# Kernel optimization log

Hardware: AMD Instinct MI355X
Metric: run time of the kernel (lower is better)

The kernel has to match this reference:

```python
import jax, jax.numpy as jnp
import numpy as np
from jax import lax

R, BS, NATM, NORB = 2, 128, 81, 240
M_DIM = 16


def _init(key, shape, scale=0.05):
    return (jax.random.normal(key, shape) * scale).astype(jnp.float32)


def setup_inputs() -> dict:
    key = jax.random.key(0)
    ks = jax.random.split(key, 24)
    return {
        "xyz": jax.random.normal(ks[0], (R, BS, NATM, 3), jnp.float32) * 3.0,
        "cn": jax.random.uniform(ks[1], (R, BS, NATM), jnp.float32),
        "edisp": jax.random.normal(ks[2], (R, BS, NATM), jnp.float32),
        "ovlp": jax.random.normal(ks[3], (R, BS, NORB, NORB), jnp.float32),
        "h0": jax.random.normal(ks[4], (R, BS, NORB, NORB), jnp.float32),
        "egfn1": jax.random.normal(ks[5], (R, BS), jnp.float32),
        "nu": jax.random.normal(ks[6], (BS, R), jnp.float32),
        # EGNN(dim=2): edge_input_dim = 2*dim + 1 = 5
        "We1": _init(ks[7], (10, 5)), "be1": jnp.zeros((10,), jnp.float32),
        "We2": _init(ks[8], (M_DIM, 10)), "be2": jnp.zeros((M_DIM,), jnp.float32),
        "Wc1": _init(ks[9], (M_DIM * 4, M_DIM)), "bc1": jnp.zeros((M_DIM * 4,), jnp.float32),
        "Wc2": _init(ks[10], (1, M_DIM * 4)), "bc2": jnp.zeros((1,), jnp.float32),
        "coors_scale": jnp.full((1,), 1e-2, jnp.float32),
        "Wn1": _init(ks[11], (4, 2 + M_DIM)), "bn1": jnp.zeros((4,), jnp.float32),
        "Wn2": _init(ks[12], (2, 4)), "bn2": jnp.zeros((2,), jnp.float32),
        "conv1_w": _init(ks[13], (2, 1, 2, 2), 0.2), "conv1_b": jnp.zeros((2,), jnp.float32),
        "conv2_w": _init(ks[14], (2, 2, 2, 2), 0.2), "conv2_b": jnp.zeros((2,), jnp.float32),
        "fc1_w": _init(ks[15], (60, 14087), 0.01), "fc1_b": jnp.zeros((60,), jnp.float32),
        "fc2_w": _init(ks[16], (30, 60)), "fc2_b": jnp.zeros((30,), jnp.float32),
        "fc3_w": _init(ks[17], (1, 30)), "fc3_b": jnp.zeros((1,), jnp.float32),
    }


def _egnn(feats, coors, We1, be1, We2, be2, Wc1, bc1, Wc2, bc2, scale, Wn1, bn1, Wn2, bn2):
    # feats: (b, n, 2), coors: (b, n, 3); dense all-pairs EGNN layer (lucidrains defaults)
    b, n, d = feats.shape
    rel = coors[:, :, None, :] - coors[:, None, :, :]            # (b, i, j, 3)
    rel_dist = jnp.sum(rel * rel, axis=-1, keepdims=True)        # (b, i, j, 1) squared dist
    fi = jnp.broadcast_to(feats[:, :, None, :], (b, n, n, d))
    fj = jnp.broadcast_to(feats[:, None, :, :], (b, n, n, d))
    edge_in = jnp.concatenate([fi, fj, rel_dist], axis=-1)       # (b, i, j, 5)
    m = jax.nn.silu(edge_in @ We1.T + be1)
    m = jax.nn.silu(m @ We2.T + be2)                             # (b, i, j, M_DIM)
    cw = (jax.nn.silu(m @ Wc1.T + bc1) @ Wc2.T + bc2)[..., 0]    # (b, i, j)
    # CoorsNorm: unit-normalize rel coords, learned scale (init 1e-2)
    norm = jnp.sqrt(jnp.clip(rel_dist, 1e-16, None))
    rel_n = rel / norm * scale
    coors_out = jnp.einsum('bij,bijc->bic', cw, rel_n) + coors
    m_i = jnp.sum(m, axis=2)                                     # sum pooling over j
    node_in = jnp.concatenate([feats, m_i], axis=-1)
    feats_out = jax.nn.silu(node_in @ Wn1.T + bn1) @ Wn2.T + bn2 + feats
    return feats_out, coors_out


def _maxpool2(x):
    return lax.reduce_window(x, -jnp.inf, lax.max, (1, 1, 2, 2), (1, 1, 2, 2), 'VALID')


def _conv_block(x, w1, b1, w2, b2):
    # x: (b, N, N) -> NCHW conv stack matching conv1/pool/conv2/pool
    x = x[:, None, :, :]
    x = lax.conv_general_dilated(x, w1, (1, 1), 'VALID', dimension_numbers=('NCHW', 'OIHW', 'NCHW'))
    x = _maxpool2(jax.nn.leaky_relu(x + b1[None, :, None, None]))
    x = lax.conv_general_dilated(x, w2, (1, 1), 'VALID', dimension_numbers=('NCHW', 'OIHW', 'NCHW'))
    x = _maxpool2(jax.nn.leaky_relu(x + b2[None, :, None, None]))
    return x


def reference(xyz, cn, edisp, ovlp, h0, egfn1, nu,
              We1, be1, We2, be2, Wc1, bc1, Wc2, bc2, coors_scale,
              Wn1, bn1, Wn2, bn2, conv1_w, conv1_b, conv2_w, conv2_b,
              fc1_w, fc1_b, fc2_w, fc2_b, fc3_w, fc3_b):
    contribs = []
    for i in range(R):  # fixed small reactant list, mirrors the Python loop
        feats = jnp.stack([cn[i], edisp[i]], axis=-1)            # (bs, n_atms, 2)
        atm, _ = _egnn(feats, xyz[i], We1, be1, We2, be2, Wc1, bc1, Wc2, bc2,
                       coors_scale, Wn1, bn1, Wn2, bn2)
        o = _conv_block(ovlp[i], conv1_w, conv1_b, conv2_w, conv2_b)
        h = _conv_block(h0[i], conv1_w, conv1_b, conv2_w, conv2_b)
        x = jnp.concatenate([o, h], axis=1).reshape(o.shape[0], -1)   # (bs, 4*59*59)
        x = jnp.concatenate([x, atm.reshape(atm.shape[0], -1), egfn1[i][:, None]], axis=1)
        x = jax.nn.leaky_relu(x @ fc1_w.T + fc1_b)
        x = jax.nn.leaky_relu(x @ fc2_w.T + fc2_b)
        x = x @ fc3_w.T + fc3_b                                   # (bs, 1)
        contribs.append(x * nu[:, i][:, None])
    return jnp.sum(jnp.concatenate(contribs, axis=1), axis=1)    # (bs,)
```

## Files before the change

### kernel.cpp

```cpp
#include <hip/hip_runtime.h>
#include <hip/hip_bf16.h>

#define XDIM 14087
#define NATM 81
#define BS   128
#define KC   128
#define NKCH 111

__device__ __forceinline__ float fast_rcp(float x) {
    return __builtin_amdgcn_rcpf(x);
}
__device__ __forceinline__ float silu(float z) {
    return z * fast_rcp(1.f + __expf(-z));
}
__device__ __forceinline__ float leaky(float z) {
    return (z > 0.f) ? z : 0.01f * z;
}

__global__ __launch_bounds__(512) void egnn_kernel(
    const float* __restrict__ xyz, const float* __restrict__ cn,
    const float* __restrict__ edisp, const float* __restrict__ egfn1,
    const float* __restrict__ We1, const float* __restrict__ be1,
    const float* __restrict__ We2, const float* __restrict__ be2,
    const float* __restrict__ Wn1, const float* __restrict__ bn1,
    const float* __restrict__ Wn2, const float* __restrict__ bn2,
    float* __restrict__ xbuf)
{
    const int bid = blockIdx.x;
    const int tid = threadIdx.x;

    __shared__ float sc[NATM][3];
    __shared__ float sf[NATM][2];
    __shared__ float sai[NATM][10];
    __shared__ float sbj[NATM][10];
    __shared__ float sW2[160];
    __shared__ float sbe2[16];
    __shared__ float sw5[10];
    __shared__ float sWn1[72];
    __shared__ float sbn1[4];
    __shared__ float sWn2[8];
    __shared__ float sbn2[2];
    __shared__ float smp[3][NATM][17];

    const float* xb = xyz + (size_t)bid * NATM * 3;
    for (int idx = tid; idx < NATM * 3; idx += 512) sc[idx / 3][idx % 3] = xb[idx];
    if (tid < NATM) {
        const float f0 = cn[(size_t)bid * NATM + tid];
        const float f1 = edisp[(size_t)bid * NATM + tid];
        sf[tid][0] = f0; sf[tid][1] = f1;
        #pragma unroll
        for (int k = 0; k < 10; ++k) {
            sai[tid][k] = be1[k] + We1[k * 5 + 0] * f0 + We1[k * 5 + 1] * f1;
            sbj[tid][k] =          We1[k * 5 + 2] * f0 + We1[k * 5 + 3] * f1;
        }
    }
    if (tid < 160) sW2[tid] = We2[tid];
    if (tid < 16)  sbe2[tid] = be2[tid];
    if (tid < 10)  sw5[tid] = We1[tid * 5 + 4];
    if (tid < 72)  sWn1[tid] = Wn1[tid];
    if (tid < 4)   sbn1[tid] = bn1[tid];
    if (tid < 8)   sWn2[tid] = Wn2[tid];
    if (tid < 2)   sbn2[tid] = bn2[tid];
    __syncthreads();

    if (tid < 486) {
        const int i    = tid % 81;
        const int part = (tid / 81) % 3;
        const int half = tid / 243;

        float W2r[80];
        #pragma unroll
        for (int q = 0; q < 80; ++q) W2r[q] = sW2[half * 80 + q];
        float be2r[8];
        #pragma unroll
        for (int q = 0; q < 8; ++q) be2r[q] = sbe2[half * 8 + q];
        float w5r[10];
        #pragma unroll
        for (int k = 0; k < 10; ++k) w5r[k] = sw5[k];
        float air[10];
        #pragma unroll
        for (int k = 0; k < 10; ++k) air[k] = sai[i][k];
        const float ci0 = sc[i][0], ci1 = sc[i][1], ci2 = sc[i][2];

        float macc[8];
        #pragma unroll
        for (int q = 0; q < 8; ++q) macc[q] = 0.f;

        const int j0 = part * 27;
        for (int j = j0; j < j0 + 27; ++j) {
            const float dx = ci0 - sc[j][0];
            const float dy = ci1 - sc[j][1];
            const float dz = ci2 - sc[j][2];
            const float rd = dx * dx + dy * dy + dz * dz;
            float h[10];
            #pragma unroll
            for (int k = 0; k < 10; ++k) {
                const float z = air[k] + sbj[j][k] + w5r[k] * rd;
                h[k] = silu(z);
            }
            #pragma unroll
            for (int q = 0; q < 8; ++q) {
                float z = be2r[q];
                #pragma unroll
                for (int k = 0; k < 10; ++k) z += W2r[q * 10 + k] * h[k];
                macc[q] += silu(z);
            }
        }
        #pragma unroll
        for (int q = 0; q < 8; ++q) smp[part][i][half * 8 + q] = macc[q];
    }
    __syncthreads();

    if (tid < NATM) {
        float mi[16];
        #pragma unroll
        for (int q = 0; q < 16; ++q)
            mi[q] = smp[0][tid][q] + smp[1][tid][q] + smp[2][tid][q];
        const float f0 = sf[tid][0], f1 = sf[tid][1];
        float n1[4];
        #pragma unroll
        for (int k = 0; k < 4; ++k) {
            float z = sbn1[k] + sWn1[k * 18 + 0] * f0 + sWn1[k * 18 + 1] * f1;
            #pragma unroll
            for (int q = 0; q < 16; ++q) z += sWn1[k * 18 + 2 + q] * mi[q];
            n1[k] = silu(z);
        }
        float* xrow = xbuf + (size_t)bid * XDIM + 13924 + tid * 2;
        #pragma unroll
        for (int c = 0; c < 2; ++c) {
            float z = sbn2[c] + (c ? f1 : f0);
            #pragma unroll
            for (int k = 0; k < 4; ++k) z += sWn2[c * 4 + k] * n1[k];
            xrow[c] = z;
        }
    }
    if (tid == 0) xbuf[(size_t)bid * XDIM + 14086] = egfn1[bid];
}

__global__ __launch_bounds__(256) void conv_kernel(
    const float* __restrict__ ovlp, const float* __restrict__ h0,
    const float* __restrict__ w1, const float* __restrict__ b1,
    const float* __restrict__ w2, const float* __restrict__ b2,
    float* __restrict__ xbuf)
{
    const int bid   = blockIdx.x;
    const int strip = bid % 15;
    const int img   = bid / 15;
    const int b     = img & 127;
    const int t     = (img >> 7) & 1;
    const int r     = img >> 8;
    const int tid   = threadIdx.x;

    const int wv = tid >> 6;
    const int l  = tid & 63;
    const int y  = strip * 4 + wv;
    if (y >= 59) return;
    const int x  = l;
    const int xc = (x < 59) ? x : 59;

    const float* src = (t ? h0 : ovlp) + (size_t)(r * BS + b) * 57600;

    float w1r[8], w2r[16], b1r[2], b2r[2];
    #pragma unroll
    for (int k = 0; k < 8; ++k) w1r[k] = w1[k];
    #pragma unroll
    for (int k = 0; k < 16; ++k) w2r[k] = w2[k];
    b1r[0] = b1[0]; b1r[1] = b1[1];
    b2r[0] = b2[0]; b2r[1] = b2[1];

    float P[7][5];
    #pragma unroll
    for (int rr = 0; rr < 7; ++rr) {
        const float* rp = src + (4 * y + rr) * 240 + 4 * xc;
        const float4 a = *reinterpret_cast<const float4*>(rp);
        P[rr][0] = a.x; P[rr][1] = a.y; P[rr][2] = a.z; P[rr][3] = a.w;
        P[rr][4] = rp[4];
    }

    float p1o[2][3][2];
    #pragma unroll
    for (int c = 0; c < 2; ++c) {
        const float wa = w1r[c * 4 + 0], wb = w1r[c * 4 + 1];
        const float wc = w1r[c * 4 + 2], wd = w1r[c * 4 + 3];
        const float bb = b1r[c];
        #pragma unroll
        for (int pr = 0; pr < 3; ++pr)
        #pragma unroll
        for (int pc = 0; pc < 2; ++pc) {
            float mx = -3.4e38f;
            #pragma unroll
            for (int s = 0; s < 2; ++s)
            #pragma unroll
            for (int tt = 0; tt < 2; ++tt) {
                const int u = 2 * pr + s, v = 2 * pc + tt;
                const float raw = fmaf(wa, P[u][v], fmaf(wb, P[u][v + 1],
                                  fmaf(wc, P[u + 1][v], fmaf(wd, P[u + 1][v + 1], bb))));
                mx = fmaxf(mx, raw);
            }
            p1o[c][pr][pc] = leaky(mx);
        }
    }

    float p1[2][3][3];
    #pragma unroll
    for (int c = 0; c < 2; ++c)
    #pragma unroll
    for (int pr = 0; pr < 3; ++pr) {
        p1[c][pr][0] = p1o[c][pr][0];
        p1[c][pr][1] = p1o[c][pr][1];
        p1[c][pr][2] = __shfl_down(p1o[c][pr][0], 1);
    }

    if (x < 59) {
        float* xrow = xbuf + (size_t)(r * BS + b) * XDIM + (size_t)(t * 2) * 3481
                      + y * 59 + x;
        #pragma unroll
        for (int c2 = 0; c2 < 2; ++c2) {
            float mx = -3.4e38f;
            #pragma unroll
            for (int a2 = 0; a2 < 2; ++a2)
            #pragma unroll
            for (int b2i = 0; b2i < 2; ++b2i) {
                float acc = b2r[c2];
                #pragma unroll
                for (int c1 = 0; c1 < 2; ++c1)
                #pragma unroll
                for (int du = 0; du < 2; ++du)
                #pragma unroll
                for (int dv = 0; dv < 2; ++dv)
                    acc += w2r[((c2 * 2 + c1) * 2 + du) * 2 + dv]
                         * p1[c1][a2 + du][b2i + dv];
                mx = fmaxf(mx, acc);
            }
            xrow[(size_t)c2 * 3481] = leaky(mx);
        }
    }
}

__global__ __launch_bounds__(256) void gemm_fc1_kernel(
    const float* __restrict__ xbuf, const float* __restrict__ fc1w,
    float* __restrict__ psum)
{
    const int kc   = blockIdx.x;
    const int mt   = blockIdx.y;
    const int tid  = threadIdx.x;
    const int kbase = kc * KC;
    const int rem   = min(KC, XDIM - kbase);
    const int row0  = mt * 32;

    __shared__ float4 X4[32][33];
    __shared__ float4 W4[64][33];

    float* Xs = reinterpret_cast<float*>(&X4[0][0]);
    float* Ws = reinterpret_cast<float*>(&W4[0][0]);

    for (int idx = tid; idx < 32 * KC; idx += 256) {
        const int m = idx >> 7, k = idx & 127;
        Xs[m * 132 + k] = (k < rem) ? xbuf[(size_t)(row0 + m) * XDIM + kbase + k] : 0.f;
    }
    for (int idx = tid; idx < 64 * KC; idx += 256) {
        const int n = idx >> 7, k = idx & 127;
        Ws[n * 132 + k] = (n < 60 && k < rem) ? fc1w[(size_t)n * XDIM + kbase + k] : 0.f;
    }
    __syncthreads();

    const int ty = tid >> 4, tx = tid & 15;
    const int m0 = ty * 2;

    float acc[2][4];
    #pragma unroll
    for (int i = 0; i < 2; ++i)
    #pragma unroll
    for (int j = 0; j < 4; ++j) acc[i][j] = 0.f;

    #pragma unroll 4
    for (int k4 = 0; k4 < 32; ++k4) {
        const float4 xa = X4[m0][k4];
        const float4 xb = X4[m0 + 1][k4];
        #pragma unroll
        for (int j = 0; j < 4; ++j) {
            const float4 w = W4[tx + 16 * j][k4];
            acc[0][j] += xa.x * w.x + xa.y * w.y + xa.z * w.z + xa.w * w.w;
            acc[1][j] += xb.x * w.x + xb.y * w.y + xb.z * w.z + xb.w * w.w;
        }
    }

    float* po = psum + ((size_t)kc * 256 + row0) * 64;
    #pragma unroll
    for (int i = 0; i < 2; ++i)
    #pragma unroll
    for (int j = 0; j < 4; ++j)
        po[(size_t)(m0 + i) * 64 + tx + 16 * j] = acc[i][j];
}

__global__ __launch_bounds__(512) void fc_tail_kernel(
    const float* __restrict__ psum,
    const float* __restrict__ fc1b,
    const float* __restrict__ fc2w, const float* __restrict__ fc2b,
    const float* __restrict__ fc3w, const float* __restrict__ fc3b,
    const float* __restrict__ nu, float* __restrict__ out)
{
    const int b = blockIdx.x;
    const int tid = threadIdx.x;
    const int n  = tid & 63;
    const int kq = (tid >> 6) & 3;
    const int rh = tid >> 8;

    __shared__ float red[2][4][64];
    __shared__ float y1s[2][64];
    __shared__ float y2s[2][30];

    const int row = rh * 128 + b;
    float s = 0.f;
    for (int kcc = kq; kcc < NKCH; kcc += 4)
        s += psum[((size_t)kcc * 256 + row) * 64 + n];
    red[rh][kq][n] = s;
    __syncthreads();

    if (kq == 0) {
        float t = red[rh][0][n] + red[rh][1][n] + red[rh][2][n] + red[rh][3][n];
        y1s[rh][n] = (n < 60) ? leaky(t + fc1b[n]) : 0.f;
    }
    __syncthreads();

    if (kq == 0 && n < 30) {
        float a2 = fc2b[n];
        const float* wr = fc2w + n * 60;
        #pragma unroll
        for (int k = 0; k < 60; ++k) a2 += wr[k] * y1s[rh][k];
        y2s[rh][n] = leaky(a2);
    }
    __syncthreads();

    if (tid == 0) {
        float acc_out = 0.f;
        #pragma unroll
        for (int r = 0; r < 2; ++r) {
            float a3 = fc3b[0];
            #pragma unroll
            for (int k = 0; k < 30; ++k) a3 += fc3w[k] * y2s[r][k];
            acc_out += a3 * nu[b * 2 + r];
        }
        out[b] = acc_out;
    }
}

extern "C" void kernel_launch(void* const* d_in, const int* in_sizes, int n_in,
                              void* d_out, int out_size, void* d_ws, size_t ws_size,
                              hipStream_t stream)
{
    const float* xyz   = (const float*)d_in[0];
    const float* cn    = (const float*)d_in[1];
    const float* edisp = (const float*)d_in[2];
    const float* ovlp  = (const float*)d_in[3];
    const float* h0    = (const float*)d_in[4];
    const float* egfn1 = (const float*)d_in[5];
    const float* nu    = (const float*)d_in[6];
    const float* We1   = (const float*)d_in[7];
    const float* be1   = (const float*)d_in[8];
    const float* We2   = (const float*)d_in[9];
    const float* be2   = (const float*)d_in[10];
    const float* Wn1   = (const float*)d_in[16];
    const float* bn1   = (const float*)d_in[17];
    const float* Wn2   = (const float*)d_in[18];
    const float* bn2   = (const float*)d_in[19];
    const float* c1w   = (const float*)d_in[20];
    const float* c1b   = (const float*)d_in[21];
    const float* c2w   = (const float*)d_in[22];
    const float* c2b   = (const float*)d_in[23];
    const float* fc1w  = (const float*)d_in[24];
    const float* fc1b  = (const float*)d_in[25];
    const float* fc2w  = (const float*)d_in[26];
    const float* fc2b  = (const float*)d_in[27];
    const float* fc3w  = (const float*)d_in[28];
    const float* fc3b  = (const float*)d_in[29];

    float* xbuf = (float*)d_ws;
    float* psum = (float*)((char*)d_ws + 14425088);
    float* out  = (float*)d_out;

    hipLaunchKernelGGL(egnn_kernel, dim3(256), dim3(512), 0, stream,
                       xyz, cn, edisp, egfn1, We1, be1, We2, be2,
                       Wn1, bn1, Wn2, bn2, xbuf);
    hipLaunchKernelGGL(conv_kernel, dim3(2 * 2 * BS * 15), dim3(256), 0, stream,
                       ovlp, h0, c1w, c1b, c2w, c2b, xbuf);
    hipLaunchKernelGGL(gemm_fc1_kernel, dim3(NKCH, 8), dim3(256), 0, stream,
                       xbuf, fc1w, psum);
    hipLaunchKernelGGL(fc_tail_kernel, dim3(128), dim3(512), 0, stream,
                       psum, fc1b, fc2w, fc2b, fc3w, fc3b, nu, out);
}
```

Measured before the change: 272.4 us.

## Pad activation rows, use direct global-to-LDS loads with XOR swizzle, two rows per conv wave

New measurement: 248.7 us. 1.1x faster.

```diff
diff --git a/kernel.cpp b/kernel.cpp
--- a/kernel.cpp
+++ b/kernel.cpp
@@ -2,6 +2,7 @@
 #include <hip/hip_bf16.h>
 
 #define XDIM 14087
+#define XPAD 14208
 #define NATM 81
 #define BS   128
 #define KC   128
@@ -15,6 +16,19 @@
 }
 __device__ __forceinline__ float leaky(float z) {
     return (z > 0.f) ? z : 0.01f * z;
+}
+
+__device__ __forceinline__ void gload_lds16(const float* g, float* l) {
+    __builtin_amdgcn_global_load_lds(
+        (const __attribute__((address_space(1))) unsigned int*)g,
+        (__attribute__((address_space(3))) unsigned int*)l, 16, 0, 0);
+}
+
+__global__ __launch_bounds__(128) void padzero_kernel(float* __restrict__ xbuf) {
+    const int row = blockIdx.x;
+    const int tid = threadIdx.x;
+    if (tid < XPAD - XDIM)
+        xbuf[(size_t)row * XPAD + XDIM + tid] = 0.f;
 }
 
 __global__ __launch_bounds__(512) void egnn_kernel(
@@ -125,7 +139,7 @@
             for (int q = 0; q < 16; ++q) z += sWn1[k * 18 + 2 + q] * mi[q];
             n1[k] = silu(z);
         }
-        float* xrow = xbuf + (size_t)bid * XDIM + 13924 + tid * 2;
+        float* xrow = xbuf + (size_t)bid * XPAD + 13924 + tid * 2;
         #pragma unroll
         for (int c = 0; c < 2; ++c) {
             float z = sbn2[c] + (c ? f1 : f0);
@@ -134,7 +148,7 @@
             xrow[c] = z;
         }
     }
-    if (tid == 0) xbuf[(size_t)bid * XDIM + 14086] = egfn1[bid];
+    if (tid == 0) xbuf[(size_t)bid * XPAD + 14086] = egfn1[bid];
 }
 
 __global__ __launch_bounds__(256) void conv_kernel(
@@ -144,8 +158,8 @@
     float* __restrict__ xbuf)
 {
     const int bid   = blockIdx.x;
-    const int strip = bid % 15;
-    const int img   = bid / 15;
+    const int strip = bid & 7;
+    const int img   = bid >> 3;
     const int b     = img & 127;
     const int t     = (img >> 7) & 1;
     const int r     = img >> 8;
@@ -153,8 +167,8 @@
 
     const int wv = tid >> 6;
     const int l  = tid & 63;
-    const int y  = strip * 4 + wv;
-    if (y >= 59) return;
+    const int y0 = strip * 8 + wv * 2;
+    if (y0 >= 59) return;
     const int x  = l;
     const int xc = (x < 59) ? x : 59;
 
@@ -168,23 +182,26 @@
     b1r[0] = b1[0]; b1r[1] = b1[1];
     b2r[0] = b2[0]; b2r[1] = b2[1];
 
-    float P[7][5];
-    #pragma unroll
-    for (int rr = 0; rr < 7; ++rr) {
-        const float* rp = src + (4 * y + rr) * 240 + 4 * xc;
-        const float4 a = *reinterpret_cast<const float4*>(rp);
+    float P[11][5];
+    #pragma unroll
+    for (int rr = 0; rr < 11; ++rr) {
+        int gr = 4 * y0 + rr;
+        if (gr > 239) gr = 239;
+        const float4 a = *reinterpret_cast<const float4*>(src + gr * 240 + 4 * xc);
         P[rr][0] = a.x; P[rr][1] = a.y; P[rr][2] = a.z; P[rr][3] = a.w;
-        P[rr][4] = rp[4];
-    }
-
-    float p1o[2][3][2];
+    }
+    #pragma unroll
+    for (int rr = 0; rr < 11; ++rr)
+        P[rr][4] = __shfl_down(P[rr][0], 1);
+
+    float p1o[2][5][2];
     #pragma unroll
     for (int c = 0; c < 2; ++c) {
         const float wa = w1r[c * 4 + 0], wb = w1r[c * 4 + 1];
         const float wc = w1r[c * 4 + 2], wd = w1r[c * 4 + 3];
         const float bb = b1r[c];
         #pragma unroll
-        for (int pr = 0; pr < 3; ++pr)
+        for (int pr = 0; pr < 5; ++pr)
         #pragma unroll
         for (int pc = 0; pc < 2; ++pc) {
             float mx = -3.4e38f;
@@ -201,38 +218,43 @@
         }
     }
 
-    float p1[2][3][3];
+    float p1[2][5][3];
     #pragma unroll
     for (int c = 0; c < 2; ++c)
     #pragma unroll
-    for (int pr = 0; pr < 3; ++pr) {
+    for (int pr = 0; pr < 5; ++pr) {
         p1[c][pr][0] = p1o[c][pr][0];
         p1[c][pr][1] = p1o[c][pr][1];
         p1[c][pr][2] = __shfl_down(p1o[c][pr][0], 1);
     }
 
-    if (x < 59) {
-        float* xrow = xbuf + (size_t)(r * BS + b) * XDIM + (size_t)(t * 2) * 3481
-                      + y * 59 + x;
-        #pragma unroll
-        for (int c2 = 0; c2 < 2; ++c2) {
-            float mx = -3.4e38f;
-            #pragma unroll
-            for (int a2 = 0; a2 < 2; ++a2)
-            #pragma unroll
-            for (int b2i = 0; b2i < 2; ++b2i) {
-                float acc = b2r[c2];
+    #pragma unroll
+    for (int oy = 0; oy < 2; ++oy) {
+        const int y = y0 + oy;
+        if (y >= 59) break;
+        if (x < 59) {
+            float* xrow = xbuf + (size_t)(r * BS + b) * XPAD + (size_t)(t * 2) * 3481
+                          + y * 59 + x;
+            #pragma unroll
+            for (int c2 = 0; c2 < 2; ++c2) {
+                float mx = -3.4e38f;
                 #pragma unroll
-                for (int c1 = 0; c1 < 2; ++c1)
+                for (int a2 = 0; a2 < 2; ++a2)
                 #pragma unroll
-                for (int du = 0; du < 2; ++du)
-                #pragma unroll
-                for (int dv = 0; dv < 2; ++dv)
-                    acc += w2r[((c2 * 2 + c1) * 2 + du) * 2 + dv]
-                         * p1[c1][a2 + du][b2i + dv];
-                mx = fmaxf(mx, acc);
+                for (int b2i = 0; b2i < 2; ++b2i) {
+                    float acc = b2r[c2];
+                    #pragma unroll
+                    for (int c1 = 0; c1 < 2; ++c1)
+                    #pragma unroll
+                    for (int du = 0; du < 2; ++du)
+                    #pragma unroll
+                    for (int dv = 0; dv < 2; ++dv)
+                        acc += w2r[((c2 * 2 + c1) * 2 + du) * 2 + dv]
+                             * p1[c1][2 * oy + a2 + du][b2i + dv];
+                    mx = fmaxf(mx, acc);
+                }
+                xrow[(size_t)c2 * 3481] = leaky(mx);
             }
-            xrow[(size_t)c2 * 3481] = leaky(mx);
         }
     }
 }
@@ -244,28 +266,46 @@
     const int kc   = blockIdx.x;
     const int mt   = blockIdx.y;
     const int tid  = threadIdx.x;
+    const int w    = tid >> 6;
+    const int l    = tid & 63;
     const int kbase = kc * KC;
-    const int rem   = min(KC, XDIM - kbase);
     const int row0  = mt * 32;
 
-    __shared__ float4 X4[32][33];
-    __shared__ float4 W4[64][33];
-
-    float* Xs = reinterpret_cast<float*>(&X4[0][0]);
-    float* Ws = reinterpret_cast<float*>(&W4[0][0]);
-
-    for (int idx = tid; idx < 32 * KC; idx += 256) {
-        const int m = idx >> 7, k = idx & 127;
-        Xs[m * 132 + k] = (k < rem) ? xbuf[(size_t)(row0 + m) * XDIM + kbase + k] : 0.f;
-    }
-    for (int idx = tid; idx < 64 * KC; idx += 256) {
-        const int n = idx >> 7, k = idx & 127;
-        Ws[n * 132 + k] = (n < 60 && k < rem) ? fc1w[(size_t)n * XDIM + kbase + k] : 0.f;
-    }
-    __syncthreads();
+    __shared__ __align__(16) float Xs[32 * 128];
+    __shared__ __align__(16) float Ws[64 * 128];
+
+    const int ml  = l >> 5;
+    const int k4s = l & 31;
+    #pragma unroll
+    for (int i = 0; i < 4; ++i) {
+        const int s  = w * 4 + i;
+        const int m  = s * 2 + ml;
+        const int k4 = k4s ^ (m & 31);
+        gload_lds16(xbuf + (size_t)(row0 + m) * XPAD + kbase + k4 * 4,
+                    Xs + s * 256);
+    }
+    const float* gmax = fc1w + ((size_t)60 * XDIM - 4);
+    #pragma unroll
+    for (int i = 0; i < 8; ++i) {
+        const int s  = w * 8 + i;
+        const int n  = s * 2 + ml;
+        const int k4 = k4s ^ (n & 31);
+        const float* g = fc1w + (size_t)n * XDIM + kbase + k4 * 4;
+        if (g > gmax) g = gmax;
+        gload_lds16(g, Ws + s * 256);
+    }
+    __syncthreads();
+
+    if (kc == NKCH - 1) {
+        if (tid < 3) Ws[7656 + tid] = fc1w[(size_t)59 * XDIM + 14084 + tid];
+        if (tid == 3) Ws[7659] = 0.f;
+        __syncthreads();
+    }
 
     const int ty = tid >> 4, tx = tid & 15;
     const int m0 = ty * 2;
+    const float4* X4 = reinterpret_cast<const float4*>(Xs);
+    const float4* W4 = reinterpret_cast<const float4*>(Ws);
 
     float acc[2][4];
     #pragma unroll
@@ -275,13 +315,14 @@
 
     #pragma unroll 4
     for (int k4 = 0; k4 < 32; ++k4) {
-        const float4 xa = X4[m0][k4];
-        const float4 xb = X4[m0 + 1][k4];
+        const float4 xa = X4[m0 * 32 + (k4 ^ m0)];
+        const float4 xb = X4[(m0 + 1) * 32 + (k4 ^ (m0 + 1))];
         #pragma unroll
         for (int j = 0; j < 4; ++j) {
-            const float4 w = W4[tx + 16 * j][k4];
-            acc[0][j] += xa.x * w.x + xa.y * w.y + xa.z * w.z + xa.w * w.w;
-            acc[1][j] += xb.x * w.x + xb.y * w.y + xb.z * w.z + xb.w * w.w;
+            const int n = tx + 16 * j;
+            const float4 wv4 = W4[n * 32 + (k4 ^ (n & 31))];
+            acc[0][j] += xa.x * wv4.x + xa.y * wv4.y + xa.z * wv4.z + xa.w * wv4.w;
+            acc[1][j] += xb.x * wv4.x + xb.y * wv4.y + xb.z * wv4.z + xb.w * wv4.w;
         }
     }
 
@@ -318,8 +359,8 @@
     __syncthreads();
 
     if (kq == 0) {
-        float t = red[rh][0][n] + red[rh][1][n] + red[rh][2][n] + red[rh][3][n];
-        y1s[rh][n] = (n < 60) ? leaky(t + fc1b[n]) : 0.f;
+        float tt = red[rh][0][n] + red[rh][1][n] + red[rh][2][n] + red[rh][3][n];
+        y1s[rh][n] = (n < 60) ? leaky(tt + fc1b[n]) : 0.f;
     }
     __syncthreads();
 
@@ -376,13 +417,14 @@
     const float* fc3b  = (const float*)d_in[29];
 
     float* xbuf = (float*)d_ws;
-    float* psum = (float*)((char*)d_ws + 14425088);
+    float* psum = (float*)((char*)d_ws + (size_t)256 * XPAD * 4);
     float* out  = (float*)d_out;
 
+    hipLaunchKernelGGL(padzero_kernel, dim3(256), dim3(128), 0, stream, xbuf);
     hipLaunchKernelGGL(egnn_kernel, dim3(256), dim3(512), 0, stream,
                        xyz, cn, edisp, egfn1, We1, be1, We2, be2,
                        Wn1, bn1, Wn2, bn2, xbuf);
-    hipLaunchKernelGGL(conv_kernel, dim3(2 * 2 * BS * 15), dim3(256), 0, stream,
+    hipLaunchKernelGGL(conv_kernel, dim3(512 * 8), dim3(256), 0, stream,
                        ovlp, h0, c1w, c1b, c2w, c2b, xbuf);
     hipLaunchKernelGGL(gemm_fc1_kernel, dim3(NKCH, 8), dim3(256), 0, stream,
                        xbuf, fc1w, psum);
```
